# Kernel optimization log

Measured on AMD Instinct MI355X. Metric: run time of the kernel, lower is better.

## Reference

```python
import jax, jax.numpy as jnp
import numpy as np

LMAX, MMAX = 4, 2
C_SPH = 32           # sphere_channels
H = 128              # edge hidden channels
N_SPECIES = 90
RESCALE = 5.0
M_SIZE_0 = LMAX + 1                                   # 5
NUM_COEFFS = sum(2 * min(l, MMAX) + 1 for l in range(LMAX + 1))  # 19
K_FULL = (LMAX + 1) ** 2                              # 25
N_NODES = 20000
N_EDGES = 320000
D_EDGE = 128
EPS = 1e-6


def layer_norm(x, scale, bias):
    mu = jnp.mean(x, axis=-1, keepdims=True)
    var = jnp.mean(jnp.square(x - mu), axis=-1, keepdims=True)
    return (x - mu) * jax.lax.rsqrt(var + EPS) * scale + bias


def setup_inputs() -> dict:
    key = jax.random.key(0)
    ks = jax.random.split(key, 12)
    node_species = jax.random.randint(ks[0], (N_NODES,), 0, N_SPECIES)
    edge_embeds = jax.random.normal(ks[1], (N_EDGES, D_EDGE), dtype=jnp.float32)
    senders = jax.random.randint(ks[2], (N_EDGES,), 0, N_NODES)
    receivers = jax.random.randint(ks[3], (N_EDGES,), 0, N_NODES)
    wigner_inv = jax.random.normal(ks[4], (N_EDGES, K_FULL, NUM_COEFFS), dtype=jnp.float32)
    # learned params
    embed_table = jax.random.normal(ks[5], (N_SPECIES, 2 * H), dtype=jnp.float32) * 0.001
    d_in = D_EDGE + 2 * H  # concat(edge, sender_emb, receiver_emb)
    W0 = jax.random.normal(ks[6], (d_in, H), dtype=jnp.float32) / np.sqrt(d_in)
    b0 = jnp.zeros((H,), jnp.float32)
    ln0_s = jnp.ones((H,), jnp.float32); ln0_b = jnp.zeros((H,), jnp.float32)
    W1 = jax.random.normal(ks[7], (H, H), dtype=jnp.float32) / np.sqrt(H)
    b1 = jnp.zeros((H,), jnp.float32)
    ln1_s = jnp.ones((H,), jnp.float32); ln1_b = jnp.zeros((H,), jnp.float32)
    W2 = jax.random.normal(ks[8], (H, M_SIZE_0 * C_SPH), dtype=jnp.float32) / np.sqrt(H)
    b2 = jnp.zeros((M_SIZE_0 * C_SPH,), jnp.float32)
    return dict(node_species=node_species, edge_embeds=edge_embeds, senders=senders,
                receivers=receivers, wigner_inv=wigner_inv, embed_table=embed_table,
                W0=W0, b0=b0, ln0_s=ln0_s, ln0_b=ln0_b,
                W1=W1, b1=b1, ln1_s=ln1_s, ln1_b=ln1_b, W2=W2, b2=b2)


def reference(node_species, edge_embeds, senders, receivers, wigner_inv, embed_table,
              W0, b0, ln0_s, ln0_b, W1, b1, ln1_s, ln1_b, W2, b2):
    num_nodes = node_species.shape[0]
    # atom edge embedding: gather + split
    node_emb = embed_table[node_species]                       # [N, 2H]
    s_emb, r_emb = jnp.split(node_emb, 2, axis=-1)             # [N, H] each
    x = jnp.concatenate((edge_embeds, s_emb[senders], r_emb[receivers]), axis=-1)  # [E, D+2H]
    # MLP with layer norm + silu between layers
    x = jax.nn.silu(layer_norm(x @ W0 + b0, ln0_s, ln0_b))
    x = jax.nn.silu(layer_norm(x @ W1 + b1, ln1_s, ln1_b))
    x = x @ W2 + b2                                            # [E, m0*C]
    feats_m_0 = x.reshape(-1, M_SIZE_0, C_SPH)                 # [E, 5, C]
    pad = jnp.zeros((x.shape[0], NUM_COEFFS - M_SIZE_0, C_SPH), dtype=x.dtype)
    edge_feats = jnp.concatenate((feats_m_0, pad), axis=1)     # [E, 19, C]
    # inverse wigner rotation back to full SH basis: [E, 25, C]
    edge_feats = jnp.einsum('ekm,emc->ekc', wigner_inv, edge_feats)
    node_feats = jax.ops.segment_sum(edge_feats, receivers, num_segments=num_nodes)
    return node_feats / RESCALE
```

## Files before the change

kernel.cpp:

```cpp
#include <hip/hip_runtime.h>
#include <hip/hip_bf16.h>
#include <cstddef>


#define MB 64
#define MTHREADS 512
#define DIN 384
#define HDIM 128
#define NOUT 160
#define NKF 25
#define WIG_LD 19
#define WIG_ROW 475

#define XS_B   784
#define FS_B   528
#define HS_B   272
#define REG0   0
#define REG1   50176
#define METAS  67584
#define METAR  67840
#define LDSSZ  68096

typedef __attribute__((ext_vector_type(8))) short short8;
typedef __attribute__((ext_vector_type(4))) float f32x4;

struct BF4 { __hip_bfloat162 a, b; };

__device__ __forceinline__ unsigned short f2bf(float f)
{
    union { float f; unsigned u; } x; x.f = f;
    unsigned r = x.u + 0x7fffu + ((x.u >> 16) & 1u);
    return (unsigned short)(r >> 16);
}

__global__ void repack_w(const float* __restrict__ W0, const float* __restrict__ W1,
                         const float* __restrict__ W2, unsigned short* __restrict__ Wp)
{
    const int id = blockIdx.x * 256 + threadIdx.x;
    const float* W; int k, n, NT, N; size_t base;
    if (id < 49152)      { W = W0; k = id >> 7;  n = id & 127;  NT = 8;  N = 128; base = 0; }
    else if (id < 65536) { int r = id - 49152; W = W1; k = r >> 7; n = r & 127; NT = 8; N = 128; base = 98304; }
    else if (id < 86016) { int r = id - 65536; W = W2; k = r / 160; n = r - 160 * k; NT = 10; N = 160; base = 131072; }
    else return;
    const float w = W[(size_t)k * N + n];
    const unsigned short hi = f2bf(w);
    union { unsigned u; float f; } hf; hf.u = ((unsigned)hi) << 16;
    const unsigned short lo = f2bf(w - hf.f);
    const int kt = k >> 5, kk = k & 31;
    const int l = ((kk >> 3) << 4) | (n & 15);
    const int i = kk & 7;
    const int nt = n >> 4;
    const size_t o = base + (size_t)((kt * NT + nt) * 2) * 512 + l * 8 + i;
    Wp[o] = hi;
    Wp[o + 512] = lo;
}

__device__ __forceinline__ void gemm_tiles(const char* __restrict__ ldsA, int astride,
                                           const char* __restrict__ wp, int NT, int KT,
                                           int nt, int lane, f32x4 acc[4])
{
    const int lr = lane & 15, lk = lane >> 4;
    for (int kt = 0; kt < KT; ++kt) {
        const char* wb = wp + (size_t)((kt * NT + nt) * 2) * 1024 + lane * 16;
        const short8 bh = *(const short8*)(wb);
        const short8 bl = *(const short8*)(wb + 1024);
        short8 a[4];
#pragma unroll
        for (int mt = 0; mt < 4; ++mt)
            a[mt] = *(const short8*)(ldsA + (mt * 16 + lr) * astride + kt * 64 + lk * 16);
#pragma unroll
        for (int mt = 0; mt < 4; ++mt) {
            acc[mt] = __builtin_amdgcn_mfma_f32_16x16x32_bf16(a[mt], bh, acc[mt], 0, 0, 0);
            acc[mt] = __builtin_amdgcn_mfma_f32_16x16x32_bf16(a[mt], bl, acc[mt], 0, 0, 0);
        }
    }
}

__device__ __forceinline__ void dump_acc(char* Hf, int nt, int lane, const f32x4 acc[4],
                                         const float bias)
{
    const int lr = lane & 15, lk = lane >> 4;
#pragma unroll
    for (int mt = 0; mt < 4; ++mt)
#pragma unroll
        for (int i = 0; i < 4; ++i)
            *(float*)(Hf + (mt * 16 + lk * 4 + i) * FS_B + (nt * 16 + lr) * 4) = acc[mt][i] + bias;
}

__device__ __forceinline__ void ln_silu_bf(const char* Hf, char* Hb,
                                           const float* __restrict__ s,
                                           const float* __restrict__ b, int t)
{
    const int j = t & 7;
    const int r = t >> 3;
    float v[16];
    float sum = 0.f, sq = 0.f;
#pragma unroll
    for (int q4 = 0; q4 < 4; ++q4) {
        const float4 x4 = *(const float4*)(Hf + r * FS_B + (j * 16 + q4 * 4) * 4);
        v[q4 * 4 + 0] = x4.x; v[q4 * 4 + 1] = x4.y;
        v[q4 * 4 + 2] = x4.z; v[q4 * 4 + 3] = x4.w;
    }
#pragma unroll
    for (int q = 0; q < 16; ++q) { sum += v[q]; sq = fmaf(v[q], v[q], sq); }
#pragma unroll
    for (int m = 1; m < 8; m <<= 1) {
        sum += __shfl_xor(sum, m, 64);
        sq  += __shfl_xor(sq,  m, 64);
    }
    const float mu = sum * (1.f / 128.f);
    const float var = sq * (1.f / 128.f) - mu * mu;
    const float rstd = rsqrtf(var + 1e-6f);
#pragma unroll
    for (int q = 0; q < 16; q += 2) {
        const int c0 = j * 16 + q;
        float y0 = (v[q] - mu) * rstd * s[c0] + b[c0];
        float y1 = (v[q + 1] - mu) * rstd * s[c0 + 1] + b[c0 + 1];
        y0 = y0 / (1.f + __expf(-y0));
        y1 = y1 / (1.f + __expf(-y1));
        *(__hip_bfloat162*)(Hb + r * HS_B + c0 * 2) =
            __float22bfloat162_rn(make_float2(y0, y1));
    }
}

__global__ __launch_bounds__(MTHREADS, 4)
void mlp_mfma(
    const int* __restrict__ species,
    const float* __restrict__ edge_embeds,
    const int* __restrict__ senders,
    const int* __restrict__ receivers,
    const float* __restrict__ embed_table,
    const char* __restrict__ Wp,
    const float* __restrict__ b0, const float* __restrict__ ln0s, const float* __restrict__ ln0b,
    const float* __restrict__ b1, const float* __restrict__ ln1s, const float* __restrict__ ln1b,
    const float* __restrict__ b2,
    float* __restrict__ F,
    int n_edges)
{
    __shared__ alignas(16) char lds[LDSSZ];
    int* sS = (int*)(lds + METAS);
    int* rS = (int*)(lds + METAR);

    const int t = threadIdx.x;
    const int e0 = blockIdx.x * MB;
    const int w = t >> 6;
    const int lane = t & 63;
    const int lr = lane & 15, lk = lane >> 4;

    if (t < MB) {
        const int e = e0 + t;
        int s = 0, r = 0;
        if (e < n_edges) { s = senders[e]; r = receivers[e]; }
        sS[t] = species[s];
        rS[t] = species[r];
    }
    __syncthreads();

    {
        const int row = t >> 3;
        const int e = e0 + row;
        const bool ev = e < n_edges;
        const int ss = sS[row], rr = rS[row];
        char* xrow = lds + REG0 + row * XS_B;
        const int c0 = (t & 7) * 4;
#pragma unroll
        for (int jj = 0; jj < 12; ++jj) {
            const int col = c0 + 32 * jj;
            float4 v = make_float4(0.f, 0.f, 0.f, 0.f);
            if (ev) {
                if (jj < 4)
                    v = *(const float4*)(edge_embeds + (size_t)e * 128 + col);
                else if (jj < 8)
                    v = *(const float4*)(embed_table + (size_t)ss * 256 + (col - 128));
                else
                    v = *(const float4*)(embed_table + (size_t)rr * 256 + 128 + (col - 256));
            }
            BF4 pk;
            pk.a = __float22bfloat162_rn(make_float2(v.x, v.y));
            pk.b = __float22bfloat162_rn(make_float2(v.z, v.w));
            *(BF4*)(xrow + col * 2) = pk;
        }
    }
    __syncthreads();

    const char* wp0 = Wp;
    const char* wp1 = Wp + 196608;
    const char* wp2 = Wp + 262144;

    f32x4 acc[4];

#pragma unroll
    for (int mt = 0; mt < 4; ++mt) acc[mt] = (f32x4){0.f, 0.f, 0.f, 0.f};
    gemm_tiles(lds + REG0, XS_B, wp0, 8, 12, w, lane, acc);
    __syncthreads();
    dump_acc(lds + REG0, w, lane, acc, b0[w * 16 + lr]);
    __syncthreads();
    ln_silu_bf(lds + REG0, lds + REG1, ln0s, ln0b, t);
    __syncthreads();

#pragma unroll
    for (int mt = 0; mt < 4; ++mt) acc[mt] = (f32x4){0.f, 0.f, 0.f, 0.f};
    gemm_tiles(lds + REG1, HS_B, wp1, 8, 4, w, lane, acc);
    dump_acc(lds + REG0, w, lane, acc, b1[w * 16 + lr]);
    __syncthreads();
    ln_silu_bf(lds + REG0, lds + REG1, ln1s, ln1b, t);
    __syncthreads();

#pragma unroll
    for (int p = 0; p < 2; ++p) {
        const int nt = w + 8 * p;
        if (nt >= 10) break;
#pragma unroll
        for (int mt = 0; mt < 4; ++mt) acc[mt] = (f32x4){0.f, 0.f, 0.f, 0.f};
        gemm_tiles(lds + REG1, HS_B, wp2, 10, 4, nt, lane, acc);
        const float bb = b2[nt * 16 + lr];
#pragma unroll
        for (int mt = 0; mt < 4; ++mt)
#pragma unroll
            for (int i = 0; i < 4; ++i) {
                const int e = e0 + mt * 16 + lk * 4 + i;
                if (e < n_edges)
                    F[(size_t)e * NOUT + nt * 16 + lr] = (acc[mt][i] + bb) * 0.2f;
            }
    }
}

__global__ void hist_kernel(const int* __restrict__ recv, int* __restrict__ cnt, int n_edges)
{
    const int e = blockIdx.x * 256 + threadIdx.x;
    if (e < n_edges) atomicAdd(&cnt[recv[e]], 1);
}

#define SCAN_T 1024
#define SCAN_CH 20
__global__ __launch_bounds__(SCAN_T)
void scan_kernel(const int* __restrict__ cnt, int* __restrict__ offsets, int n_nodes)
{
    __shared__ int waveSum[SCAN_T / 64];
    const int t = threadIdx.x;
    const int base = t * SCAN_CH;
    int local[SCAN_CH];
    int s = 0;
#pragma unroll
    for (int j = 0; j < SCAN_CH; ++j) {
        const int v = (base + j < n_nodes) ? cnt[base + j] : 0;
        local[j] = s;
        s += v;
    }
    const int lane = t & 63;
    int incl = s;
#pragma unroll
    for (int d = 1; d < 64; d <<= 1) {
        const int u = __shfl_up(incl, d, 64);
        if (lane >= d) incl += u;
    }
    if (lane == 63) waveSum[t >> 6] = incl;
    __syncthreads();
    if (t < SCAN_T / 64) {
        const int v = waveSum[t];
        int incl2 = v;
#pragma unroll
        for (int d = 1; d < SCAN_T / 64; d <<= 1) {
            const int u = __shfl_up(incl2, d, 64);
            if (lane >= d) incl2 += u;
        }
        waveSum[t] = incl2 - v;
    }
    __syncthreads();
    const int threadExcl = waveSum[t >> 6] + (incl - s);
#pragma unroll
    for (int j = 0; j < SCAN_CH; ++j)
        if (base + j < n_nodes) offsets[base + j] = threadExcl + local[j];
    if (t == SCAN_T - 1) offsets[n_nodes] = threadExcl + s;
}

__global__ void scatter_kernel(const int* __restrict__ recv, int* __restrict__ cursor,
                               int* __restrict__ elist, int n_edges)
{
    const int e = blockIdx.x * 256 + threadIdx.x;
    if (e < n_edges) {
        const int p = atomicAdd(&cursor[recv[e]], 1);
        elist[p] = e;
    }
}

__global__ __launch_bounds__(256)
void agg_kernel(const float* __restrict__ wigner, const float* __restrict__ F,
                const int* __restrict__ offsets, const int* __restrict__ elist,
                float* __restrict__ out)
{
    const int n = blockIdx.x;
    const int t = threadIdx.x;
    __shared__ float wigS[2][128];

    const int beg = offsets[n];
    const int end = offsets[n + 1];

    const int ch = t & 31;
    const int k0 = t >> 5;
    float a0 = 0.f, a1 = 0.f, a2 = 0.f, a3 = 0.f;

    float f[5];
    if (beg < end) {
        const int e = elist[beg];
        if (t < 125) wigS[0][t] = wigner[(size_t)e * WIG_ROW + (t / 5) * WIG_LD + (t % 5)];
        const float* Fp = F + (size_t)e * NOUT + ch;
#pragma unroll
        for (int m = 0; m < 5; ++m) f[m] = Fp[m * 32];
    }

    int buf = 0;
    for (int i = beg; i < end; ++i) {
        __syncthreads();
        float fc[5];
#pragma unroll
        for (int m = 0; m < 5; ++m) fc[m] = f[m];
        if (i + 1 < end) {
            const int e = elist[i + 1];
            if (t < 125) wigS[buf ^ 1][t] = wigner[(size_t)e * WIG_ROW + (t / 5) * WIG_LD + (t % 5)];
            const float* Fp = F + (size_t)e * NOUT + ch;
#pragma unroll
            for (int m = 0; m < 5; ++m) f[m] = Fp[m * 32];
        }
        const float* wp = &wigS[buf][0];
        { const float* wq = wp + k0 * 5;        a0 += wq[0]*fc[0] + wq[1]*fc[1] + wq[2]*fc[2] + wq[3]*fc[3] + wq[4]*fc[4]; }
        { const float* wq = wp + (k0 + 8) * 5;  a1 += wq[0]*fc[0] + wq[1]*fc[1] + wq[2]*fc[2] + wq[3]*fc[3] + wq[4]*fc[4]; }
        { const float* wq = wp + (k0 + 16) * 5; a2 += wq[0]*fc[0] + wq[1]*fc[1] + wq[2]*fc[2] + wq[3]*fc[3] + wq[4]*fc[4]; }
        if (t < 32) { const float* wq = wp + 120; a3 += wq[0]*fc[0] + wq[1]*fc[1] + wq[2]*fc[2] + wq[3]*fc[3] + wq[4]*fc[4]; }
        buf ^= 1;
    }

    float* orow = out + (size_t)n * (NKF * 32);
    orow[t] = a0;
    orow[t + 256] = a1;
    orow[t + 512] = a2;
    if (t < 32) orow[t + 768] = a3;
}

#define EB 32
__device__ __forceinline__ void ln_silu_f(float (*Bx)[HDIM], const float* __restrict__ s,
                                          const float* __restrict__ b, int t)
{
    const int r = t >> 3;
    const int j = t & 7;
    float v[16];
    float sum = 0.f, sq = 0.f;
#pragma unroll
    for (int q = 0; q < 16; ++q) { v[q] = Bx[r][j*16+q]; sum += v[q]; sq = fmaf(v[q], v[q], sq); }
#pragma unroll
    for (int m = 1; m < 8; m <<= 1) { sum += __shfl_xor(sum, m, 64); sq += __shfl_xor(sq, m, 64); }
    const float mu = sum * (1.f/HDIM);
    const float var = sq * (1.f/HDIM) - mu*mu;
    const float rstd = rsqrtf(var + 1e-6f);
#pragma unroll
    for (int q = 0; q < 16; ++q) {
        const int cc = j*16+q;
        const float y = (v[q]-mu)*rstd*s[cc]+b[cc];
        Bx[r][cc] = y / (1.f + __expf(-y));
    }
}

__global__ __launch_bounds__(256, 2)
void edge_fused_kernel(
    const int* __restrict__ species, const float* __restrict__ edge_embeds,
    const int* __restrict__ senders, const int* __restrict__ receivers,
    const float* __restrict__ wigner, const float* __restrict__ embed_table,
    const float* __restrict__ W0, const float* __restrict__ b0,
    const float* __restrict__ ln0s, const float* __restrict__ ln0b,
    const float* __restrict__ W1, const float* __restrict__ b1,
    const float* __restrict__ ln1s, const float* __restrict__ ln1b,
    const float* __restrict__ W2, const float* __restrict__ b2,
    float* __restrict__ out, int n_edges)
{
    __shared__ float A[EB][DIN];
    __shared__ float Bx[EB][HDIM];
    __shared__ int sSpec[EB], rSpec[EB], rNode[EB];
    const int t = threadIdx.x;
    const int e0 = blockIdx.x * EB;
    if (t < EB) {
        const int e = e0 + t;
        int s = 0, r = 0;
        if (e < n_edges) { s = senders[e]; r = receivers[e]; }
        sSpec[t] = species[s]; rSpec[t] = species[r]; rNode[t] = r;
    }
    __syncthreads();
    for (int idx = t; idx < EB * DIN; idx += 256) {
        const int r = idx / DIN;
        const int i = idx - r * DIN;
        const int e = e0 + r;
        float v = 0.f;
        if (e < n_edges) {
            if (i < HDIM) v = edge_embeds[(size_t)e * HDIM + i];
            else if (i < 2*HDIM) v = embed_table[(size_t)sSpec[r]*256 + (i-HDIM)];
            else v = embed_table[(size_t)rSpec[r]*256 + HDIM + (i-2*HDIM)];
        }
        A[r][i] = v;
    }
    __syncthreads();
    const int c = t & (HDIM-1);
    const int g = t >> 7;
    float acc[16];
#pragma unroll
    for (int q = 0; q < 16; ++q) acc[q] = 0.f;
    for (int it = 0; it < DIN/4; ++it) {
        const float wa = W0[(4*it+0)*HDIM+c], wb = W0[(4*it+1)*HDIM+c];
        const float wc = W0[(4*it+2)*HDIM+c], wd = W0[(4*it+3)*HDIM+c];
#pragma unroll
        for (int q = 0; q < 16; ++q) {
            const float4 x4 = *reinterpret_cast<const float4*>(&A[g*16+q][4*it]);
            acc[q] = fmaf(x4.x, wa, fmaf(x4.y, wb, fmaf(x4.z, wc, fmaf(x4.w, wd, acc[q]))));
        }
    }
    { const float bb = b0[c];
#pragma unroll
      for (int q = 0; q < 16; ++q) Bx[g*16+q][c] = acc[q] + bb; }
    __syncthreads(); ln_silu_f(Bx, ln0s, ln0b, t); __syncthreads();
#pragma unroll
    for (int q = 0; q < 16; ++q) acc[q] = 0.f;
    for (int it = 0; it < HDIM/4; ++it) {
        const float wa = W1[(4*it+0)*HDIM+c], wb = W1[(4*it+1)*HDIM+c];
        const float wc = W1[(4*it+2)*HDIM+c], wd = W1[(4*it+3)*HDIM+c];
#pragma unroll
        for (int q = 0; q < 16; ++q) {
            const float4 x4 = *reinterpret_cast<const float4*>(&Bx[g*16+q][4*it]);
            acc[q] = fmaf(x4.x, wa, fmaf(x4.y, wb, fmaf(x4.z, wc, fmaf(x4.w, wd, acc[q]))));
        }
    }
    __syncthreads();
    { const float bb = b1[c];
#pragma unroll
      for (int q = 0; q < 16; ++q) Bx[g*16+q][c] = acc[q] + bb; }
    __syncthreads(); ln_silu_f(Bx, ln1s, ln1b, t); __syncthreads();
    float* Ff = &A[0][0];
    {
        float a2[16];
#pragma unroll
        for (int q = 0; q < 16; ++q) a2[q] = 0.f;
        for (int it = 0; it < HDIM/4; ++it) {
            const float wa = W2[(4*it+0)*NOUT+c], wb = W2[(4*it+1)*NOUT+c];
            const float wc = W2[(4*it+2)*NOUT+c], wd = W2[(4*it+3)*NOUT+c];
#pragma unroll
            for (int q = 0; q < 16; ++q) {
                const float4 x4 = *reinterpret_cast<const float4*>(&Bx[g*16+q][4*it]);
                a2[q] = fmaf(x4.x, wa, fmaf(x4.y, wb, fmaf(x4.z, wc, fmaf(x4.w, wd, a2[q]))));
            }
        }
        const float bb = b2[c];
#pragma unroll
        for (int q = 0; q < 16; ++q) Ff[(g*16+q)*NOUT+c] = (a2[q]+bb)*0.2f;
    }
    {
        const int c2 = HDIM + (t & 31);
        const int g8 = t >> 5;
        float a2[4] = {0.f, 0.f, 0.f, 0.f};
        for (int it = 0; it < HDIM/4; ++it) {
            const float wa = W2[(4*it+0)*NOUT+c2], wb = W2[(4*it+1)*NOUT+c2];
            const float wc = W2[(4*it+2)*NOUT+c2], wd = W2[(4*it+3)*NOUT+c2];
#pragma unroll
            for (int q = 0; q < 4; ++q) {
                const float4 x4 = *reinterpret_cast<const float4*>(&Bx[g8*4+q][4*it]);
                a2[q] = fmaf(x4.x, wa, fmaf(x4.y, wb, fmaf(x4.z, wc, fmaf(x4.w, wd, a2[q]))));
            }
        }
        const float bb = b2[c2];
#pragma unroll
        for (int q = 0; q < 4; ++q) Ff[(g8*4+q)*NOUT+c2] = (a2[q]+bb)*0.2f;
    }
    __syncthreads();
    for (int r = 0; r < EB; ++r) {
        const int e = e0 + r;
        if (e >= n_edges) break;
        const float* wrow = wigner + (size_t)e * WIG_ROW;
        float* orow = out + (size_t)rNode[r] * (NKF*32);
        const float* Fr = Ff + r * NOUT;
#pragma unroll
        for (int jj = 0; jj < 4; ++jj) {
            const int p = t + 256*jj;
            if (p < NKF*32) {
                const int k = p >> 5, chh = p & 31;
                float val = 0.f;
#pragma unroll
                for (int m = 0; m < 5; ++m)
                    val = fmaf(wrow[k*WIG_LD+m], Fr[m*32+chh], val);
                atomicAdd(&orow[p], val);
            }
        }
    }
}

extern "C" void kernel_launch(void* const* d_in, const int* in_sizes, int n_in,
                              void* d_out, int out_size, void* d_ws, size_t ws_size,
                              hipStream_t stream)
{
    const int*   species     = (const int*)d_in[0];
    const float* edge_embeds = (const float*)d_in[1];
    const int*   senders     = (const int*)d_in[2];
    const int*   receivers   = (const int*)d_in[3];
    const float* wigner      = (const float*)d_in[4];
    const float* embed_table = (const float*)d_in[5];
    const float* W0 = (const float*)d_in[6];
    const float* b0 = (const float*)d_in[7];
    const float* ln0s = (const float*)d_in[8];
    const float* ln0b = (const float*)d_in[9];
    const float* W1 = (const float*)d_in[10];
    const float* b1 = (const float*)d_in[11];
    const float* ln1s = (const float*)d_in[12];
    const float* ln1b = (const float*)d_in[13];
    const float* W2 = (const float*)d_in[14];
    const float* b2 = (const float*)d_in[15];
    float* out = (float*)d_out;

    const int n_nodes = in_sizes[0];
    const int n_edges = in_sizes[2];

    const size_t wpBytes   = 344064;
    const size_t fBytes    = (size_t)n_edges * NOUT * sizeof(float);
    const size_t offBytes  = (size_t)(n_nodes + 1) * sizeof(int);
    const size_t curBytes  = (size_t)n_nodes * sizeof(int);
    const size_t listBytes = (size_t)n_edges * sizeof(int);
    const size_t need = wpBytes + fBytes + offBytes + curBytes + listBytes + 64;

    if (ws_size < need || n_nodes > SCAN_T * SCAN_CH) {
        hipMemsetAsync(out, 0, (size_t)out_size * sizeof(float), stream);
        const int nblocks = (n_edges + EB - 1) / EB;
        hipLaunchKernelGGL(edge_fused_kernel, dim3(nblocks), dim3(256), 0, stream,
                           species, edge_embeds, senders, receivers, wigner, embed_table,
                           W0, b0, ln0s, ln0b, W1, b1, ln1s, ln1b, W2, b2, out, n_edges);
        return;
    }

    char* ws = (char*)d_ws;
    unsigned short* Wp = (unsigned short*)ws;
    float* F       = (float*)(ws + wpBytes);
    int*   offsets = (int*)(ws + wpBytes + fBytes);
    int*   cursor  = (int*)(ws + wpBytes + fBytes + offBytes);
    int*   elist   = (int*)(ws + wpBytes + fBytes + offBytes + curBytes);

    const int egrid = (n_edges + 255) / 256;

    hipLaunchKernelGGL(repack_w, dim3(336), dim3(256), 0, stream, W0, W1, W2, Wp);

    hipMemsetAsync(cursor, 0, curBytes, stream);
    hipLaunchKernelGGL(hist_kernel, dim3(egrid), dim3(256), 0, stream,
                       receivers, cursor, n_edges);
    hipLaunchKernelGGL(scan_kernel, dim3(1), dim3(SCAN_T), 0, stream,
                       cursor, offsets, n_nodes);
    hipMemcpyAsync(cursor, offsets, curBytes, hipMemcpyDeviceToDevice, stream);
    hipLaunchKernelGGL(scatter_kernel, dim3(egrid), dim3(256), 0, stream,
                       receivers, cursor, elist, n_edges);

    const int mblocks = (n_edges + MB - 1) / MB;
    hipLaunchKernelGGL(mlp_mfma, dim3(mblocks), dim3(MTHREADS), 0, stream,
                       species, edge_embeds, senders, receivers, embed_table,
                       (const char*)Wp, b0, ln0s, ln0b, b1, ln1s, ln1b, b2, F, n_edges);

    hipLaunchKernelGGL(agg_kernel, dim3(n_nodes), dim3(256), 0, stream,
                       wigner, F, offsets, elist, out);
}
```

Measured before the change: 527.5 us.

## Halve MLP edge tile, 2x2 wave tiling, fuse cursor copy, shrink aggregation block

The MLP kernel now handles 32 edges per block with 256 threads. Each wave computes two N-tiles by two M-tiles, so every A fragment read from LDS is reused across two weight tiles, and the smaller LDS footprint should allow more resident blocks. The scan kernel writes the cursor array directly, which removes a device-to-device memcpy. The aggregation kernel drops to 128 threads per node, each accumulating up to 7 output rows. The risks are more blocks re-reading the weights, lower occupancy per block in aggregation, and aliasing of the scan's input and cursor pointers despite `__restrict__`.

```diff
diff --git a/kernel.cpp b/kernel.cpp
--- a/kernel.cpp
+++ b/kernel.cpp
@@ -3,8 +3,8 @@
 #include <cstddef>
 
 
-#define MB 64
-#define MTHREADS 512
+#define MB 32
+#define MTHREADS 256
 #define DIN 384
 #define HDIM 128
 #define NOUT 160
@@ -12,14 +12,18 @@
 #define WIG_LD 19
 #define WIG_ROW 475
 
+#define WP1OFF 196608
+#define WP2OFF 262144
+#define WPBYTES 344064
+
 #define XS_B   784
 #define FS_B   528
 #define HS_B   272
 #define REG0   0
-#define REG1   50176
-#define METAS  67584
-#define METAR  67840
-#define LDSSZ  68096
+#define REG1   25088
+#define METAS  33792
+#define METAR  33920
+#define LDSSZ  34048
 
 typedef __attribute__((ext_vector_type(8))) short short8;
 typedef __attribute__((ext_vector_type(4))) float f32x4;
@@ -55,33 +59,58 @@
     Wp[o + 512] = lo;
 }
 
-__device__ __forceinline__ void gemm_tiles(const char* __restrict__ ldsA, int astride,
-                                           const char* __restrict__ wp, int NT, int KT,
-                                           int nt, int lane, f32x4 acc[4])
+__device__ __forceinline__ void gemm_tiles2(const char* __restrict__ ldsA, int astride,
+                                            const char* __restrict__ wp, int NT, int KT,
+                                            int nt, int lane, f32x4 acc[2])
 {
     const int lr = lane & 15, lk = lane >> 4;
     for (int kt = 0; kt < KT; ++kt) {
         const char* wb = wp + (size_t)((kt * NT + nt) * 2) * 1024 + lane * 16;
         const short8 bh = *(const short8*)(wb);
         const short8 bl = *(const short8*)(wb + 1024);
-        short8 a[4];
-#pragma unroll
-        for (int mt = 0; mt < 4; ++mt)
+        short8 a[2];
+#pragma unroll
+        for (int mt = 0; mt < 2; ++mt)
             a[mt] = *(const short8*)(ldsA + (mt * 16 + lr) * astride + kt * 64 + lk * 16);
 #pragma unroll
-        for (int mt = 0; mt < 4; ++mt) {
+        for (int mt = 0; mt < 2; ++mt) {
             acc[mt] = __builtin_amdgcn_mfma_f32_16x16x32_bf16(a[mt], bh, acc[mt], 0, 0, 0);
             acc[mt] = __builtin_amdgcn_mfma_f32_16x16x32_bf16(a[mt], bl, acc[mt], 0, 0, 0);
         }
     }
 }
 
-__device__ __forceinline__ void dump_acc(char* Hf, int nt, int lane, const f32x4 acc[4],
-                                         const float bias)
+__device__ __forceinline__ void gemm_tiles2x2(const char* __restrict__ ldsA, int astride,
+                                              const char* __restrict__ wp, int NT, int KT,
+                                              int ntbase, int lane, f32x4 acc[2][2])
 {
     const int lr = lane & 15, lk = lane >> 4;
-#pragma unroll
-    for (int mt = 0; mt < 4; ++mt)
+    for (int kt = 0; kt < KT; ++kt) {
+        short8 a[2];
+#pragma unroll
+        for (int mt = 0; mt < 2; ++mt)
+            a[mt] = *(const short8*)(ldsA + (mt * 16 + lr) * astride + kt * 64 + lk * 16);
+#pragma unroll
+        for (int p = 0; p < 2; ++p) {
+            const int nt = ntbase + 4 * p;
+            const char* wb = wp + (size_t)((kt * NT + nt) * 2) * 1024 + lane * 16;
+            const short8 bh = *(const short8*)(wb);
+            const short8 bl = *(const short8*)(wb + 1024);
+#pragma unroll
+            for (int mt = 0; mt < 2; ++mt) {
+                acc[p][mt] = __builtin_amdgcn_mfma_f32_16x16x32_bf16(a[mt], bh, acc[p][mt], 0, 0, 0);
+                acc[p][mt] = __builtin_amdgcn_mfma_f32_16x16x32_bf16(a[mt], bl, acc[p][mt], 0, 0, 0);
+            }
+        }
+    }
+}
+
+__device__ __forceinline__ void dump_acc2(char* Hf, int nt, int lane, const f32x4 acc[2],
+                                          const float bias)
+{
+    const int lr = lane & 15, lk = lane >> 4;
+#pragma unroll
+    for (int mt = 0; mt < 2; ++mt)
 #pragma unroll
         for (int i = 0; i < 4; ++i)
             *(float*)(Hf + (mt * 16 + lk * 4 + i) * FS_B + (nt * 16 + lr) * 4) = acc[mt][i] + bias;
@@ -184,43 +213,56 @@
     __syncthreads();
 
     const char* wp0 = Wp;
-    const char* wp1 = Wp + 196608;
-    const char* wp2 = Wp + 262144;
-
-    f32x4 acc[4];
-
-#pragma unroll
-    for (int mt = 0; mt < 4; ++mt) acc[mt] = (f32x4){0.f, 0.f, 0.f, 0.f};
-    gemm_tiles(lds + REG0, XS_B, wp0, 8, 12, w, lane, acc);
-    __syncthreads();
-    dump_acc(lds + REG0, w, lane, acc, b0[w * 16 + lr]);
+    const char* wp1 = Wp + WP1OFF;
+    const char* wp2 = Wp + WP2OFF;
+
+    f32x4 acc[2][2];
+
+#pragma unroll
+    for (int p = 0; p < 2; ++p)
+#pragma unroll
+        for (int mt = 0; mt < 2; ++mt) acc[p][mt] = (f32x4){0.f, 0.f, 0.f, 0.f};
+    gemm_tiles2x2(lds + REG0, XS_B, wp0, 8, 12, w, lane, acc);
+    __syncthreads();
+#pragma unroll
+    for (int p = 0; p < 2; ++p) {
+        const int nt = w + 4 * p;
+        dump_acc2(lds + REG0, nt, lane, acc[p], b0[nt * 16 + lr]);
+    }
     __syncthreads();
     ln_silu_bf(lds + REG0, lds + REG1, ln0s, ln0b, t);
     __syncthreads();
 
 #pragma unroll
-    for (int mt = 0; mt < 4; ++mt) acc[mt] = (f32x4){0.f, 0.f, 0.f, 0.f};
-    gemm_tiles(lds + REG1, HS_B, wp1, 8, 4, w, lane, acc);
-    dump_acc(lds + REG0, w, lane, acc, b1[w * 16 + lr]);
+    for (int p = 0; p < 2; ++p)
+#pragma unroll
+        for (int mt = 0; mt < 2; ++mt) acc[p][mt] = (f32x4){0.f, 0.f, 0.f, 0.f};
+    gemm_tiles2x2(lds + REG1, HS_B, wp1, 8, 4, w, lane, acc);
+#pragma unroll
+    for (int p = 0; p < 2; ++p) {
+        const int nt = w + 4 * p;
+        dump_acc2(lds + REG0, nt, lane, acc[p], b1[nt * 16 + lr]);
+    }
     __syncthreads();
     ln_silu_bf(lds + REG0, lds + REG1, ln1s, ln1b, t);
     __syncthreads();
 
 #pragma unroll
-    for (int p = 0; p < 2; ++p) {
-        const int nt = w + 8 * p;
+    for (int p = 0; p < 3; ++p) {
+        const int nt = w + 4 * p;
         if (nt >= 10) break;
-#pragma unroll
-        for (int mt = 0; mt < 4; ++mt) acc[mt] = (f32x4){0.f, 0.f, 0.f, 0.f};
-        gemm_tiles(lds + REG1, HS_B, wp2, 10, 4, nt, lane, acc);
+        f32x4 a3[2];
+#pragma unroll
+        for (int mt = 0; mt < 2; ++mt) a3[mt] = (f32x4){0.f, 0.f, 0.f, 0.f};
+        gemm_tiles2(lds + REG1, HS_B, wp2, 10, 4, nt, lane, a3);
         const float bb = b2[nt * 16 + lr];
 #pragma unroll
-        for (int mt = 0; mt < 4; ++mt)
+        for (int mt = 0; mt < 2; ++mt)
 #pragma unroll
             for (int i = 0; i < 4; ++i) {
                 const int e = e0 + mt * 16 + lk * 4 + i;
                 if (e < n_edges)
-                    F[(size_t)e * NOUT + nt * 16 + lr] = (acc[mt][i] + bb) * 0.2f;
+                    F[(size_t)e * NOUT + nt * 16 + lr] = (a3[mt][i] + bb) * 0.2f;
             }
     }
 }
@@ -234,7 +276,8 @@
 #define SCAN_T 1024
 #define SCAN_CH 20
 __global__ __launch_bounds__(SCAN_T)
-void scan_kernel(const int* __restrict__ cnt, int* __restrict__ offsets, int n_nodes)
+void scan_kernel(const int* __restrict__ cnt, int* __restrict__ offsets,
+                 int* __restrict__ cursor, int n_nodes)
 {
     __shared__ int waveSum[SCAN_T / 64];
     const int t = threadIdx.x;
@@ -270,7 +313,11 @@
     const int threadExcl = waveSum[t >> 6] + (incl - s);
 #pragma unroll
     for (int j = 0; j < SCAN_CH; ++j)
-        if (base + j < n_nodes) offsets[base + j] = threadExcl + local[j];
+        if (base + j < n_nodes) {
+            const int o = threadExcl + local[j];
+            offsets[base + j] = o;
+            cursor[base + j] = o;
+        }
     if (t == SCAN_T - 1) offsets[n_nodes] = threadExcl + s;
 }
 
@@ -284,7 +331,7 @@
     }
 }
 
-__global__ __launch_bounds__(256)
+__global__ __launch_bounds__(128)
 void agg_kernel(const float* __restrict__ wigner, const float* __restrict__ F,
                 const int* __restrict__ offsets, const int* __restrict__ elist,
                 float* __restrict__ out)
@@ -298,7 +345,9 @@
 
     const int ch = t & 31;
     const int k0 = t >> 5;
-    float a0 = 0.f, a1 = 0.f, a2 = 0.f, a3 = 0.f;
+    float a[7];
+#pragma unroll
+    for (int j = 0; j < 7; ++j) a[j] = 0.f;
 
     float f[5];
     if (beg < end) {
@@ -323,18 +372,24 @@
             for (int m = 0; m < 5; ++m) f[m] = Fp[m * 32];
         }
         const float* wp = &wigS[buf][0];
-        { const float* wq = wp + k0 * 5;        a0 += wq[0]*fc[0] + wq[1]*fc[1] + wq[2]*fc[2] + wq[3]*fc[3] + wq[4]*fc[4]; }
-        { const float* wq = wp + (k0 + 8) * 5;  a1 += wq[0]*fc[0] + wq[1]*fc[1] + wq[2]*fc[2] + wq[3]*fc[3] + wq[4]*fc[4]; }
-        { const float* wq = wp + (k0 + 16) * 5; a2 += wq[0]*fc[0] + wq[1]*fc[1] + wq[2]*fc[2] + wq[3]*fc[3] + wq[4]*fc[4]; }
-        if (t < 32) { const float* wq = wp + 120; a3 += wq[0]*fc[0] + wq[1]*fc[1] + wq[2]*fc[2] + wq[3]*fc[3] + wq[4]*fc[4]; }
+#pragma unroll
+        for (int j = 0; j < 7; ++j) {
+            const int k = k0 + 4 * j;
+            if (k < NKF) {
+                const float* wq = wp + k * 5;
+                a[j] += wq[0] * fc[0] + wq[1] * fc[1] + wq[2] * fc[2]
+                      + wq[3] * fc[3] + wq[4] * fc[4];
+            }
+        }
         buf ^= 1;
     }
 
     float* orow = out + (size_t)n * (NKF * 32);
-    orow[t] = a0;
-    orow[t + 256] = a1;
-    orow[t + 512] = a2;
-    if (t < 32) orow[t + 768] = a3;
+#pragma unroll
+    for (int j = 0; j < 7; ++j) {
+        const int k = k0 + 4 * j;
+        if (k < NKF) orow[k * 32 + ch] = a[j];
+    }
 }
 
 #define EB 32
@@ -513,14 +568,14 @@
     const int n_nodes = in_sizes[0];
     const int n_edges = in_sizes[2];
 
-    const size_t wpBytes   = 344064;
+    const size_t wpBytes   = WPBYTES;
     const size_t fBytes    = (size_t)n_edges * NOUT * sizeof(float);
     const size_t offBytes  = (size_t)(n_nodes + 1) * sizeof(int);
     const size_t curBytes  = (size_t)n_nodes * sizeof(int);
     const size_t listBytes = (size_t)n_edges * sizeof(int);
     const size_t need = wpBytes + fBytes + offBytes + curBytes + listBytes + 64;
 
-    if (ws_size < need || n_nodes > SCAN_T * SCAN_CH) {
+    if (ws_size < need || n_nodes > SCAN_T * SCAN_CH || n_edges <= 0) {
         hipMemsetAsync(out, 0, (size_t)out_size * sizeof(float), stream);
         const int nblocks = (n_edges + EB - 1) / EB;
         hipLaunchKernelGGL(edge_fused_kernel, dim3(nblocks), dim3(256), 0, stream,
@@ -544,8 +599,7 @@
     hipLaunchKernelGGL(hist_kernel, dim3(egrid), dim3(256), 0, stream,
                        receivers, cursor, n_edges);
     hipLaunchKernelGGL(scan_kernel, dim3(1), dim3(SCAN_T), 0, stream,
-                       cursor, offsets, n_nodes);
-    hipMemcpyAsync(cursor, offsets, curBytes, hipMemcpyDeviceToDevice, stream);
+                       cursor, offsets, cursor, n_nodes);
     hipLaunchKernelGGL(scatter_kernel, dim3(egrid), dim3(256), 0, stream,
                        receivers, cursor, elist, n_edges);
 
@@ -554,6 +608,6 @@
                        species, edge_embeds, senders, receivers, embed_table,
                        (const char*)Wp, b0, ln0s, ln0b, b1, ln1s, ln1b, b2, F, n_edges);
 
-    hipLaunchKernelGGL(agg_kernel, dim3(n_nodes), dim3(256), 0, stream,
+    hipLaunchKernelGGL(agg_kernel, dim3(n_nodes), dim3(128), 0, stream,
                        wigner, F, offsets, elist, out);
 }
```

After: 524.1 us. About the same (-0.6%).

## Drop split-bf16 weight compensation, prefetch B tiles, fold cursor copy into scan

Applied to the files above, without the earlier changes.

Weights are now packed as a single bf16 copy instead of a hi/lo split, which halves the MFMA count and the weight bytes in every MLP GEMM. The GEMM helper is templated on tile counts, fully unrolled, and software-prefetches the next B fragment before issuing MFMAs. Occupancy hint in launch bounds goes from 4 to 2, and the scan kernel writes the cursor array directly, removing a device-to-device memcpy. Dropping the lo term lowers weight precision to plain bf16, which risks accuracy against the fp32 reference. Also note the scan reads cnt from the same buffer it writes cursor into, which is in-place aliasing.

```diff
diff --git a/kernel.cpp b/kernel.cpp
--- a/kernel.cpp
+++ b/kernel.cpp
@@ -12,6 +12,10 @@
 #define WIG_LD 19
 #define WIG_ROW 475
 
+#define WP1OFF 98304
+#define WP2OFF 131072
+#define WPBYTES 172032
+
 #define XS_B   784
 #define FS_B   528
 #define HS_B   272
@@ -39,45 +43,42 @@
     const int id = blockIdx.x * 256 + threadIdx.x;
     const float* W; int k, n, NT, N; size_t base;
     if (id < 49152)      { W = W0; k = id >> 7;  n = id & 127;  NT = 8;  N = 128; base = 0; }
-    else if (id < 65536) { int r = id - 49152; W = W1; k = r >> 7; n = r & 127; NT = 8; N = 128; base = 98304; }
-    else if (id < 86016) { int r = id - 65536; W = W2; k = r / 160; n = r - 160 * k; NT = 10; N = 160; base = 131072; }
+    else if (id < 65536) { int r = id - 49152; W = W1; k = r >> 7; n = r & 127; NT = 8; N = 128; base = 49152; }
+    else if (id < 86016) { int r = id - 65536; W = W2; k = r / 160; n = r - 160 * k; NT = 10; N = 160; base = 65536; }
     else return;
     const float w = W[(size_t)k * N + n];
-    const unsigned short hi = f2bf(w);
-    union { unsigned u; float f; } hf; hf.u = ((unsigned)hi) << 16;
-    const unsigned short lo = f2bf(w - hf.f);
     const int kt = k >> 5, kk = k & 31;
     const int l = ((kk >> 3) << 4) | (n & 15);
     const int i = kk & 7;
     const int nt = n >> 4;
-    const size_t o = base + (size_t)((kt * NT + nt) * 2) * 512 + l * 8 + i;
-    Wp[o] = hi;
-    Wp[o + 512] = lo;
-}
-
-__device__ __forceinline__ void gemm_tiles(const char* __restrict__ ldsA, int astride,
-                                           const char* __restrict__ wp, int NT, int KT,
-                                           int nt, int lane, f32x4 acc[4])
+    Wp[base + (size_t)(kt * NT + nt) * 512 + l * 8 + i] = f2bf(w);
+}
+
+template<int NT, int KT>
+__device__ __forceinline__ void gemm_tiles4(const char* __restrict__ ldsA, int astride,
+                                            const char* __restrict__ wp,
+                                            int nt, int lane, f32x4 acc[4])
 {
     const int lr = lane & 15, lk = lane >> 4;
+    short8 bcur = *(const short8*)(wp + (size_t)nt * 1024 + lane * 16);
+#pragma unroll
     for (int kt = 0; kt < KT; ++kt) {
-        const char* wb = wp + (size_t)((kt * NT + nt) * 2) * 1024 + lane * 16;
-        const short8 bh = *(const short8*)(wb);
-        const short8 bl = *(const short8*)(wb + 1024);
+        short8 bnxt = bcur;
+        if (kt + 1 < KT)
+            bnxt = *(const short8*)(wp + (size_t)((kt + 1) * NT + nt) * 1024 + lane * 16);
         short8 a[4];
 #pragma unroll
         for (int mt = 0; mt < 4; ++mt)
             a[mt] = *(const short8*)(ldsA + (mt * 16 + lr) * astride + kt * 64 + lk * 16);
 #pragma unroll
-        for (int mt = 0; mt < 4; ++mt) {
-            acc[mt] = __builtin_amdgcn_mfma_f32_16x16x32_bf16(a[mt], bh, acc[mt], 0, 0, 0);
-            acc[mt] = __builtin_amdgcn_mfma_f32_16x16x32_bf16(a[mt], bl, acc[mt], 0, 0, 0);
-        }
-    }
-}
-
-__device__ __forceinline__ void dump_acc(char* Hf, int nt, int lane, const f32x4 acc[4],
-                                         const float bias)
+        for (int mt = 0; mt < 4; ++mt)
+            acc[mt] = __builtin_amdgcn_mfma_f32_16x16x32_bf16(a[mt], bcur, acc[mt], 0, 0, 0);
+        bcur = bnxt;
+    }
+}
+
+__device__ __forceinline__ void dump_acc4(char* Hf, int nt, int lane, const f32x4 acc[4],
+                                          const float bias)
 {
     const int lr = lane & 15, lk = lane >> 4;
 #pragma unroll
@@ -123,7 +124,7 @@
     }
 }
 
-__global__ __launch_bounds__(MTHREADS, 4)
+__global__ __launch_bounds__(MTHREADS, 2)
 void mlp_mfma(
     const int* __restrict__ species,
     const float* __restrict__ edge_embeds,
@@ -184,24 +185,24 @@
     __syncthreads();
 
     const char* wp0 = Wp;
-    const char* wp1 = Wp + 196608;
-    const char* wp2 = Wp + 262144;
+    const char* wp1 = Wp + WP1OFF;
+    const char* wp2 = Wp + WP2OFF;
 
     f32x4 acc[4];
 
 #pragma unroll
     for (int mt = 0; mt < 4; ++mt) acc[mt] = (f32x4){0.f, 0.f, 0.f, 0.f};
-    gemm_tiles(lds + REG0, XS_B, wp0, 8, 12, w, lane, acc);
-    __syncthreads();
-    dump_acc(lds + REG0, w, lane, acc, b0[w * 16 + lr]);
+    gemm_tiles4<8, 12>(lds + REG0, XS_B, wp0, w, lane, acc);
+    __syncthreads();
+    dump_acc4(lds + REG0, w, lane, acc, b0[w * 16 + lr]);
     __syncthreads();
     ln_silu_bf(lds + REG0, lds + REG1, ln0s, ln0b, t);
     __syncthreads();
 
 #pragma unroll
     for (int mt = 0; mt < 4; ++mt) acc[mt] = (f32x4){0.f, 0.f, 0.f, 0.f};
-    gemm_tiles(lds + REG1, HS_B, wp1, 8, 4, w, lane, acc);
-    dump_acc(lds + REG0, w, lane, acc, b1[w * 16 + lr]);
+    gemm_tiles4<8, 4>(lds + REG1, HS_B, wp1, w, lane, acc);
+    dump_acc4(lds + REG0, w, lane, acc, b1[w * 16 + lr]);
     __syncthreads();
     ln_silu_bf(lds + REG0, lds + REG1, ln1s, ln1b, t);
     __syncthreads();
@@ -212,7 +213,7 @@
         if (nt >= 10) break;
 #pragma unroll
         for (int mt = 0; mt < 4; ++mt) acc[mt] = (f32x4){0.f, 0.f, 0.f, 0.f};
-        gemm_tiles(lds + REG1, HS_B, wp2, 10, 4, nt, lane, acc);
+        gemm_tiles4<10, 4>(lds + REG1, HS_B, wp2, nt, lane, acc);
         const float bb = b2[nt * 16 + lr];
 #pragma unroll
         for (int mt = 0; mt < 4; ++mt)
@@ -234,7 +235,8 @@
 #define SCAN_T 1024
 #define SCAN_CH 20
 __global__ __launch_bounds__(SCAN_T)
-void scan_kernel(const int* __restrict__ cnt, int* __restrict__ offsets, int n_nodes)
+void scan_kernel(const int* __restrict__ cnt, int* __restrict__ offsets,
+                 int* __restrict__ cursor, int n_nodes)
 {
     __shared__ int waveSum[SCAN_T / 64];
     const int t = threadIdx.x;
@@ -270,7 +272,11 @@
     const int threadExcl = waveSum[t >> 6] + (incl - s);
 #pragma unroll
     for (int j = 0; j < SCAN_CH; ++j)
-        if (base + j < n_nodes) offsets[base + j] = threadExcl + local[j];
+        if (base + j < n_nodes) {
+            const int o = threadExcl + local[j];
+            offsets[base + j] = o;
+            cursor[base + j] = o;
+        }
     if (t == SCAN_T - 1) offsets[n_nodes] = threadExcl + s;
 }
 
@@ -513,14 +519,14 @@
     const int n_nodes = in_sizes[0];
     const int n_edges = in_sizes[2];
 
-    const size_t wpBytes   = 344064;
+    const size_t wpBytes   = WPBYTES;
     const size_t fBytes    = (size_t)n_edges * NOUT * sizeof(float);
     const size_t offBytes  = (size_t)(n_nodes + 1) * sizeof(int);
     const size_t curBytes  = (size_t)n_nodes * sizeof(int);
     const size_t listBytes = (size_t)n_edges * sizeof(int);
     const size_t need = wpBytes + fBytes + offBytes + curBytes + listBytes + 64;
 
-    if (ws_size < need || n_nodes > SCAN_T * SCAN_CH) {
+    if (ws_size < need || n_nodes > SCAN_T * SCAN_CH || n_edges <= 0) {
         hipMemsetAsync(out, 0, (size_t)out_size * sizeof(float), stream);
         const int nblocks = (n_edges + EB - 1) / EB;
         hipLaunchKernelGGL(edge_fused_kernel, dim3(nblocks), dim3(256), 0, stream,
@@ -544,8 +550,7 @@
     hipLaunchKernelGGL(hist_kernel, dim3(egrid), dim3(256), 0, stream,
                        receivers, cursor, n_edges);
     hipLaunchKernelGGL(scan_kernel, dim3(1), dim3(SCAN_T), 0, stream,
-                       cursor, offsets, n_nodes);
-    hipMemcpyAsync(cursor, offsets, curBytes, hipMemcpyDeviceToDevice, stream);
+                       cursor, offsets, cursor, n_nodes);
     hipLaunchKernelGGL(scatter_kernel, dim3(egrid), dim3(256), 0, stream,
                        receivers, cursor, elist, n_edges);
 
```

New measurement: 502.3 us. -4.8%, faster.
